# Kernel tuning notes

Measured on AMD Instinct MI355X. Metric: run time of the kernel, lower is better.

## Reference

```python
import jax, jax.numpy as jnp
import numpy as np

DIM = 512
HEADS = 8
HEAD_DIM = DIM // HEADS
EPS = 1e-6
LN_EPS = 1e-5


def setup_inputs() -> dict:
    key = jax.random.key(0)
    ks = jax.random.split(key, 7)
    B, S = 2, 2048
    std = 1.0 / np.sqrt(DIM)
    return {
        "x": jax.random.normal(ks[0], (B, S, DIM), dtype=jnp.float32),
        "Wq": jax.random.normal(ks[1], (DIM, DIM), dtype=jnp.float32) * std,
        "Wk": jax.random.normal(ks[2], (DIM, DIM), dtype=jnp.float32) * std,
        "Wv": jax.random.normal(ks[3], (DIM, DIM), dtype=jnp.float32) * std,
        "Wo": jax.random.normal(ks[4], (DIM, DIM), dtype=jnp.float32) * std,
        "ln_gamma": jnp.ones((DIM,), dtype=jnp.float32),
        "ln_beta": jnp.zeros((DIM,), dtype=jnp.float32),
    }


def _hardsigmoid(x):
    return jnp.clip(x / 6.0 + 0.5, 0.0, 1.0)


def _softshrink(x, lambd=0.5):
    return jnp.where(x > lambd, x - lambd, jnp.where(x < -lambd, x + lambd, 0.0))


def reference(x, Wq, Wk, Wv, Wo, ln_gamma, ln_beta):
    B, S, D = x.shape
    # torch Linear: y = x @ W.T
    q = (x @ Wq.T).reshape(B, S, HEADS, HEAD_DIM).transpose(0, 2, 1, 3)
    k = (x @ Wk.T).reshape(B, S, HEADS, HEAD_DIM).transpose(0, 2, 1, 3)
    v = (x @ Wv.T).reshape(B, S, HEADS, HEAD_DIM).transpose(0, 2, 1, 3)
    scale = 1.0 / np.sqrt(HEAD_DIM)
    scores = jnp.einsum("bhqd,bhkd->bhqk", q, k) * scale  # [B,H,S,S]
    attn_soft = jax.nn.softmax(scores, axis=-1)
    gated = attn_soft * _hardsigmoid(scores)
    attn_weights = gated / (gated.sum(axis=-1, keepdims=True) + EPS)
    attn_out = jnp.einsum("bhqk,bhkd->bhqd", attn_weights, v)
    attn_out = attn_out.transpose(0, 2, 1, 3).reshape(B, S, D)
    out = attn_out @ Wo.T
    out = out / (1.0 + jnp.abs(out))  # softsign
    out = out + _softshrink(x)
    # LayerNorm over last dim
    mu = out.mean(axis=-1, keepdims=True)
    var = ((out - mu) ** 2).mean(axis=-1, keepdims=True)
    out = (out - mu) * jax.lax.rsqrt(var + LN_EPS) * ln_gamma + ln_beta
    return out
```

## Files before the change

### kernel.cpp

```cpp
#include <hip/hip_runtime.h>

#define DIMD 512
#define NB 2
#define SEQ 2048
#define NHEADS 8
#define HDIM 64
#define MROWS (NB*SEQ)

typedef short s16x8 __attribute__((ext_vector_type(8)));
typedef float f32x4 __attribute__((ext_vector_type(4)));
typedef float f32x16 __attribute__((ext_vector_type(16)));
typedef unsigned short u16;
typedef unsigned int u32;

__device__ __forceinline__ u16 f2bf(float f) {
    union { float f; u32 u; } c; c.f = f;
    u32 u = c.u;
    return (u16)((u + 0x7FFFu + ((u >> 16) & 1u)) >> 16);
}
__device__ __forceinline__ float bf2f(u16 v) {
    union { u32 u; float f; } c; c.u = ((u32)v) << 16;
    return c.f;
}

__device__ __forceinline__ f32x4 mfma16(s16x8 a, s16x8 b, f32x4 c) {
    return __builtin_amdgcn_mfma_f32_16x16x32_bf16(a, b, c, 0, 0, 0);
}
__device__ __forceinline__ f32x16 mfma32(s16x8 a, s16x8 b, f32x16 c) {
    return __builtin_amdgcn_mfma_f32_32x32x16_bf16(a, b, c, 0, 0, 0);
}
__device__ __forceinline__ float fexp2(float x) {
    float r; asm("v_exp_f32 %0, %1" : "=v"(r) : "v"(x)); return r;
}

#define GLDS16(g, l) __builtin_amdgcn_global_load_lds( \
    (const __attribute__((address_space(1))) void*)(g), \
    (__attribute__((address_space(3))) void*)(l), 16, 0, 0)

#define ESCF 0.180336880111f
#define HSC2 0.115524530f

__global__ void cvt_all(const float* __restrict__ x, const float* __restrict__ Wq,
                        const float* __restrict__ Wk, const float* __restrict__ Wv,
                        const float* __restrict__ Wo,
                        u16* __restrict__ xb, u16* __restrict__ wqkv, u16* __restrict__ wo) {
    int i = blockIdx.x * blockDim.x + threadIdx.x;
    const float* src; u16* dst; int idx;
    if (i < 524288) { src = x; dst = xb; idx = i; }
    else {
        int jj = i - 524288;
        int which = jj >> 16; idx = jj & 65535;
        src = which == 0 ? Wq : which == 1 ? Wk : which == 2 ? Wv : Wo;
        dst = which < 3 ? wqkv + which*DIMD*DIMD : wo;
    }
    float4 v = reinterpret_cast<const float4*>(src)[idx];
    ushort4 o;
    o.x = f2bf(v.x); o.y = f2bf(v.y); o.z = f2bf(v.z); o.w = f2bf(v.w);
    reinterpret_cast<ushort4*>(dst)[idx] = o;
}

template<int WMODE>
__global__ __launch_bounds__(256) void gemm128(const u16* __restrict__ A, const u16* __restrict__ Bm,
                                               void* __restrict__ Cout, void* __restrict__ Cout2,
                                               void* __restrict__ Cout3, int M, int N, int K) {
    __shared__ u16 As[128*64];
    __shared__ u16 Bs[128*64];
    const int bm0 = blockIdx.x * 128, bn0 = blockIdx.y * 128;
    const int t = threadIdx.x;
    const int w = t >> 6, l = t & 63;
    const int lg = l >> 4, lr = l & 15;
    const int wm = w >> 1, wn = w & 1;
    f32x4 acc[4][4] = {};
    const int srow = w*32 + (l >> 3);
    const int swc = ((l & 7) ^ ((l >> 3) & 7)) * 8;
    const u16* asrc = A  + (size_t)(bm0 + srow)*K + swc;
    const u16* bsrc = Bm + (size_t)(bn0 + srow)*K + swc;
    const int ldsb = w*2048;

    for (int k0 = 0; k0 < K; k0 += 64) {
        #pragma unroll
        for (int g = 0; g < 4; g++) {
            GLDS16(asrc + (size_t)g*8*K + k0, &As[ldsb + g*512]);
            GLDS16(bsrc + (size_t)g*8*K + k0, &Bs[ldsb + g*512]);
        }
        __syncthreads();
        #pragma unroll
        for (int ks = 0; ks < 2; ks++) {
            const int swr = ((ks*4 + lg) ^ (lr & 7)) * 8;
            s16x8 af[4], bfr[4];
            #pragma unroll
            for (int fm = 0; fm < 4; fm++)
                af[fm] = *(const s16x8*)&As[(wm*64 + fm*16 + lr)*64 + swr];
            #pragma unroll
            for (int fn = 0; fn < 4; fn++)
                bfr[fn] = *(const s16x8*)&Bs[(wn*64 + fn*16 + lr)*64 + swr];
            #pragma unroll
            for (int fm = 0; fm < 4; fm++)
                #pragma unroll
                for (int fn = 0; fn < 4; fn++)
                    acc[fm][fn] = mfma16(af[fm], bfr[fn], acc[fm][fn]);
        }
        __syncthreads();
    }

    const int region = (WMODE == 3) ? (bn0 >> 9) : 0;
    const float qsc = (WMODE == 3 && region == 0) ? ESCF : 1.0f;
    #pragma unroll
    for (int fm = 0; fm < 4; fm++) {
        #pragma unroll
        for (int fn = 0; fn < 4; fn++) {
            const int mb = bm0 + wm*64 + fm*16 + lg*4;
            const int n  = bn0 + wn*64 + fn*16 + lr;
            if (WMODE == 2) {
                float* C = (float*)Cout;
                #pragma unroll
                for (int i = 0; i < 4; i++)
                    C[(size_t)(mb + i)*N + n] = acc[fm][fn][i];
            } else {
                const int nl = n & 511;
                if (region == 2) {
                    const int b = mb >> 11, s0 = mb & 2047;
                    const int h = nl >> 6, d = nl & 63;
                    ushort4 pk;
                    pk.x = f2bf(acc[fm][fn][0]);
                    pk.y = f2bf(acc[fm][fn][1]);
                    pk.z = f2bf(acc[fm][fn][2]);
                    pk.w = f2bf(acc[fm][fn][3]);
                    *(ushort4*)((u16*)Cout3 + (size_t)((b*8 + h)*64 + d)*2048 + s0) = pk;
                } else {
                    u16* C = region == 0 ? (u16*)Cout : (u16*)Cout2;
                    #pragma unroll
                    for (int i = 0; i < 4; i++)
                        C[(size_t)(mb + i)*512 + nl] = f2bf(acc[fm][fn][i] * qsc);
                }
            }
        }
    }
}

__global__ __launch_bounds__(256) void gemm_bt2(const u16* __restrict__ A, const u16* __restrict__ Bm,
                                                u16* __restrict__ Cout, int M, int N, int K) {
    __shared__ u16 As[64*64];
    __shared__ u16 Bs[64*64];
    const int bm0 = blockIdx.x * 64, bn0 = blockIdx.y * 64;
    const int t = threadIdx.x;
    const int w = t >> 6, l = t & 63;
    const int lg = l >> 4, lr = l & 15;
    const int wm = w >> 1, wn = w & 1;
    f32x4 acc[2][2] = {};
    const int srow = t >> 3;
    const int scol = (t & 7) * 8;

    for (int k0 = 0; k0 < K; k0 += 64) {
        #pragma unroll
        for (int c = 0; c < 2; c++) {
            const u16* ga = A  + (size_t)(bm0 + c*32 + srow)*K + k0 + scol;
            const u16* gb = Bm + (size_t)(bn0 + c*32 + srow)*K + k0 + scol;
            GLDS16(ga, (char*)As + c*4096 + w*1024);
            GLDS16(gb, (char*)Bs + c*4096 + w*1024);
        }
        __syncthreads();
        #pragma unroll
        for (int ks = 0; ks < 2; ks++) {
            s16x8 af[2], bfr[2];
            #pragma unroll
            for (int fm = 0; fm < 2; fm++)
                af[fm] = *(const s16x8*)&As[(wm*32 + fm*16 + lr)*64 + ks*32 + lg*8];
            #pragma unroll
            for (int fn = 0; fn < 2; fn++)
                bfr[fn] = *(const s16x8*)&Bs[(wn*32 + fn*16 + lr)*64 + ks*32 + lg*8];
            #pragma unroll
            for (int fm = 0; fm < 2; fm++)
                #pragma unroll
                for (int fn = 0; fn < 2; fn++)
                    acc[fm][fn] = mfma16(af[fm], bfr[fn], acc[fm][fn]);
        }
        __syncthreads();
    }

    #pragma unroll
    for (int fm = 0; fm < 2; fm++)
        #pragma unroll
        for (int fn = 0; fn < 2; fn++) {
            const int mb = bm0 + wm*32 + fm*16 + lg*4;
            const int n  = bn0 + wn*32 + fn*16 + lr;
            #pragma unroll
            for (int i = 0; i < 4; i++)
                Cout[(size_t)(mb + i)*N + n] = f2bf(acc[fm][fn][i]);
        }
}

__global__ __launch_bounds__(256) void attn_split(const u16* __restrict__ q, const u16* __restrict__ k,
                                                  const u16* __restrict__ vt,
                                                  u16* __restrict__ opart, float* __restrict__ gpart) {
    __shared__ u16 Ks[3][64*64];
    __shared__ u16 Vs[2][64*64];
    const int bid = blockIdx.x;
    const int xcd = bid & 7, j = bid >> 3;
    const int g8 = j >> 4, qt = j & 15;
    const int bhks = xcd*8 + g8;
    const int bh = bhks >> 2, ks = bhks & 3;
    const int b = bh >> 3, h = bh & 7;
    const int qb0 = qt * 128;
    const int t = threadIdx.x;
    const int w = t >> 6, l = t & 63;
    const int ln = l & 31, hi = l >> 5, l7 = l & 7;

    const size_t qrow = (size_t)(b*SEQ + qb0 + w*32 + ln);
    s16x8 qf[4];
    #pragma unroll
    for (int c = 0; c < 4; c++)
        qf[c] = *(const s16x8*)(q + qrow*DIMD + h*HDIM + c*16 + hi*8);

    const int sr = l >> 3;
    const int swc = ((l & 7) ^ sr) * 8;
    const u16* ksrc = k  + (size_t)(b*SEQ + ks*512 + w*16 + sr)*DIMD + h*HDIM + swc;
    const u16* vsrc = vt + (size_t)bh*HDIM*SEQ + (size_t)(w*16 + sr)*SEQ + ks*512 + swc;
    const int ldsw = w*1024;

    f32x16 o0 = {}, o1 = {};
    float gacc = 0.f;

#define SV(T, B) do { GLDS16(vsrc + (T)*64,                 &Vs[B][ldsw]); \
                      GLDS16(vsrc + (size_t)8*SEQ + (T)*64, &Vs[B][ldsw + 512]); } while(0)
#define SK(T, B) do { GLDS16(ksrc + (size_t)((T)*64)*DIMD,     &Ks[B][ldsw]); \
                      GLDS16(ksrc + (size_t)((T)*64 + 8)*DIMD, &Ks[B][ldsw + 512]); } while(0)
#define WB(N) do { asm volatile("s_waitcnt vmcnt(" #N ")" ::: "memory"); \
                   __builtin_amdgcn_s_barrier(); \
                   asm volatile("" ::: "memory"); } while(0)
#define QKH(B, KB, SC) do { SC = (f32x16){}; \
    __builtin_amdgcn_s_setprio(1); \
    _Pragma("unroll") for (int c_ = 0; c_ < 4; c_++) { \
        const int ch_ = (((c_ << 1) | hi) ^ l7) * 8; \
        s16x8 kf_ = *(const s16x8*)&Ks[B][((KB)*32 + ln)*64 + ch_]; \
        SC = mfma32(kf_, qf[c_], SC); } \
    __builtin_amdgcn_s_setprio(0); } while(0)
#define SMPV(SC, KB, VB) do { \
    u32 up_[4][2]; \
    _Pragma("unroll") for (int b2_ = 0; b2_ < 4; b2_++) { \
        const float s0_ = SC[b2_*4+0], s1_ = SC[b2_*4+1]; \
        const float s2_ = SC[b2_*4+2], s3_ = SC[b2_*4+3]; \
        const float w0_ = fexp2(s0_) * __builtin_amdgcn_fmed3f(s0_*HSC2 + 0.5f, 0.f, 1.f); \
        const float w1_ = fexp2(s1_) * __builtin_amdgcn_fmed3f(s1_*HSC2 + 0.5f, 0.f, 1.f); \
        const float w2_ = fexp2(s2_) * __builtin_amdgcn_fmed3f(s2_*HSC2 + 0.5f, 0.f, 1.f); \
        const float w3_ = fexp2(s3_) * __builtin_amdgcn_fmed3f(s3_*HSC2 + 0.5f, 0.f, 1.f); \
        gacc += (w0_ + w1_) + (w2_ + w3_); \
        asm("v_cvt_pk_bf16_f32 %0, %1, %2" : "=v"(up_[b2_][0]) : "v"(w0_), "v"(w1_)); \
        asm("v_cvt_pk_bf16_f32 %0, %1, %2" : "=v"(up_[b2_][1]) : "v"(w2_), "v"(w3_)); } \
    _Pragma("unroll") for (int c16_ = 0; c16_ < 2; c16_++) { \
        u32 x0_ = up_[2*c16_][0], y0_ = up_[2*c16_+1][0]; \
        u32 x1_ = up_[2*c16_][1], y1_ = up_[2*c16_+1][1]; \
        asm("v_permlane32_swap_b32 %0, %1" : "+v"(x0_), "+v"(y0_)); \
        asm("v_permlane32_swap_b32 %0, %1" : "+v"(x1_), "+v"(y1_)); \
        union { u32 w[4]; s16x8 v; } pa_; \
        pa_.w[0] = x0_; pa_.w[1] = x1_; pa_.w[2] = y0_; pa_.w[3] = y1_; \
        const int ccv_ = (KB)*4 + c16_*2 + hi; \
        s16x8 vf0_ = *(const s16x8*)&Vs[VB][(size_t)ln*64        + (ccv_ ^ l7)*8]; \
        s16x8 vf1_ = *(const s16x8*)&Vs[VB][(size_t)(32 + ln)*64 + (ccv_ ^ l7)*8]; \
        __builtin_amdgcn_s_setprio(1); \
        o0 = mfma32(pa_.v, vf0_, o0); \
        o1 = mfma32(pa_.v, vf1_, o1); \
        __builtin_amdgcn_s_setprio(0); } } while(0)

    f32x16 a0, a1, b0, b1;
    SV(0,0); SK(0,0); SK(1,1);
    WB(2);
    QKH(0,0,a0); SK(2,2); QKH(0,1,a1);
    WB(2);
    SV(1,1); QKH(1,0,b0); SK(3,0); SMPV(a0,0,0); QKH(1,1,b1); SMPV(a1,1,0);
    WB(2);
    SV(2,0); QKH(2,0,a0); SK(4,1); SMPV(b0,0,1); QKH(2,1,a1); SMPV(b1,1,1);
    WB(2);
    SV(3,1); QKH(0,0,b0); SK(5,2); SMPV(a0,0,0); QKH(0,1,b1); SMPV(a1,1,0);
    WB(2);
    SV(4,0); QKH(1,0,a0); SK(6,0); SMPV(b0,0,1); QKH(1,1,a1); SMPV(b1,1,1);
    WB(2);
    SV(5,1); QKH(2,0,b0); SK(7,1); SMPV(a0,0,0); QKH(2,1,b1); SMPV(a1,1,0);
    WB(2);
    SV(6,0); QKH(0,0,a0); SMPV(b0,0,1); QKH(0,1,a1); SMPV(b1,1,1);
    WB(0);
    SV(7,1); QKH(1,0,b0); SMPV(a0,0,0); QKH(1,1,b1); SMPV(a1,1,0);
    WB(0);
    SMPV(b0,0,1); SMPV(b1,1,1);

#undef SV
#undef SK
#undef WB
#undef QKH
#undef SMPV

    gacc += __shfl_xor(gacc, 32);
    if (l < 32)
        gpart[((size_t)ks*16 + bh)*SEQ + qb0 + w*32 + l] = gacc;

    u16* op = opart + ((size_t)ks*MROWS + b*SEQ + qb0 + w*32)*DIMD + h*HDIM;
    #pragma unroll
    for (int i = 0; i < 16; i++) {
        const int qr = (i & 3) + 8*(i >> 2) + 4*hi;
        op[(size_t)qr*DIMD + ln]      = f2bf(o0[i]);
        op[(size_t)qr*DIMD + 32 + ln] = f2bf(o1[i]);
    }
}

__global__ __launch_bounds__(256) void attn_combine(const u16* __restrict__ opart,
                                                    const float* __restrict__ gpart,
                                                    u16* __restrict__ attn) {
    const int idx = blockIdx.x*256 + threadIdx.x;
    const int row = idx >> 6;
    const int colb = (idx & 63) * 8;
    const int b = row >> 11, s = row & 2047, h = colb >> 6;
    float g = 0.f;
    #pragma unroll
    for (int p = 0; p < 4; p++)
        g += gpart[((size_t)p*16 + b*8 + h)*SEQ + s];
    const float inv = 1.f / g;
    float acc[8] = {};
    #pragma unroll
    for (int p = 0; p < 4; p++) {
        s16x8 v = *(const s16x8*)(opart + ((size_t)p*MROWS + row)*DIMD + colb);
        #pragma unroll
        for (int j2 = 0; j2 < 8; j2++) acc[j2] += bf2f((u16)v[j2]);
    }
    union { u16 r[8]; s16x8 v; } o;
    #pragma unroll
    for (int j2 = 0; j2 < 8; j2++) o.r[j2] = f2bf(acc[j2]*inv);
    *(s16x8*)(attn + (size_t)row*DIMD + colb) = o.v;
}

__global__ __launch_bounds__(256) void ln_epilogue(const u16* __restrict__ proj, const float* __restrict__ x,
                                                   const float* __restrict__ gamma, const float* __restrict__ beta,
                                                   float* __restrict__ out) {
    const int row = blockIdx.x*4 + (threadIdx.x >> 6);
    const int l = threadIdx.x & 63;
    const u16* pr = proj + (size_t)row*DIMD + l*8;
    const float* xr = x  + (size_t)row*DIMD + l*8;
    s16x8 pv = *(const s16x8*)pr;
    float tv[8];
    float s = 0.f, s2 = 0.f;
    #pragma unroll
    for (int j = 0; j < 2; j++) {
        float4 xv = *(const float4*)(xr + j*4);
        float xa[4] = {xv.x, xv.y, xv.z, xv.w};
        #pragma unroll
        for (int qq = 0; qq < 4; qq++) {
            const float p = bf2f((u16)pv[j*4+qq]);
            const float ss = p / (1.f + fabsf(p));
            const float xx = xa[qq];
            const float sh = xx > 0.5f ? xx - 0.5f : (xx < -0.5f ? xx + 0.5f : 0.f);
            const float tt = ss + sh;
            tv[j*4+qq] = tt; s += tt; s2 += tt*tt;
        }
    }
    #pragma unroll
    for (int m = 1; m < 64; m <<= 1) { s += __shfl_xor(s, m); s2 += __shfl_xor(s2, m); }
    const float mu = s * (1.f/512.f);
    float var = s2 * (1.f/512.f) - mu*mu;
    const float rstd = rsqrtf(var + 1e-5f);
    #pragma unroll
    for (int j = 0; j < 2; j++) {
        float4 g  = *(const float4*)(gamma + l*8 + j*4);
        float4 bb = *(const float4*)(beta  + l*8 + j*4);
        float4 ov;
        ov.x = (tv[j*4+0]-mu)*rstd*g.x + bb.x;
        ov.y = (tv[j*4+1]-mu)*rstd*g.y + bb.y;
        ov.z = (tv[j*4+2]-mu)*rstd*g.z + bb.z;
        ov.w = (tv[j*4+3]-mu)*rstd*g.w + bb.w;
        *(float4*)(out + (size_t)row*DIMD + l*8 + j*4) = ov;
    }
}

extern "C" void kernel_launch(void* const* d_in, const int* in_sizes, int n_in,
                              void* d_out, int out_size, void* d_ws, size_t ws_size,
                              hipStream_t stream) {
    const float* x     = (const float*)d_in[0];
    const float* Wq    = (const float*)d_in[1];
    const float* Wk    = (const float*)d_in[2];
    const float* Wv    = (const float*)d_in[3];
    const float* Wo    = (const float*)d_in[4];
    const float* gamma = (const float*)d_in[5];
    const float* beta  = (const float*)d_in[6];
    float* out = (float*)d_out;
    char* ws = (char*)d_ws;

    u16* xb    = (u16*)(ws);
    u16* wqkvb = (u16*)(ws + (4<<20));
    u16* wob   = (u16*)(ws + (4<<20) + (1536<<10));
    u16* qb    = (u16*)(ws + (6<<20));
    u16* kb    = (u16*)(ws + (10<<20));
    u16* vtb   = (u16*)(ws + (14<<20));
    u16* ab    = (u16*)(ws + (18<<20));
    u16* proj  = (u16*)(ws + (22<<20));
    u16* opart = (u16*)(ws + (26<<20));
    float* gpart = (float*)(ws + (42<<20));

    cvt_all<<<3072, 256, 0, stream>>>(x, Wq, Wk, Wv, Wo, xb, wqkvb, wob);

    gemm128<3><<<dim3(MROWS/128, 1536/128), 256, 0, stream>>>(xb, wqkvb, qb, kb, vtb, MROWS, 1536, DIMD);

    attn_split<<<1024, 256, 0, stream>>>(qb, kb, vtb, opart, gpart);
    attn_combine<<<1024, 256, 0, stream>>>(opart, gpart, ab);

    gemm_bt2<<<dim3(MROWS/64, DIMD/64), 256, 0, stream>>>(ab, wob, proj, MROWS, DIMD, DIMD);

    ln_epilogue<<<MROWS/4, 256, 0, stream>>>(proj, x, gamma, beta, out);
}
```

Measured before the change: 69.54 us.

## Fuse split-K attention combine into output projection GEMM A-tile load

```diff
diff --git a/kernel.cpp b/kernel.cpp
--- a/kernel.cpp
+++ b/kernel.cpp
@@ -31,6 +31,9 @@
 }
 __device__ __forceinline__ float fexp2(float x) {
     float r; asm("v_exp_f32 %0, %1" : "=v"(r) : "v"(x)); return r;
+}
+__device__ __forceinline__ float frcp(float x) {
+    float r; asm("v_rcp_f32 %0, %1" : "=v"(r) : "v"(x)); return r;
 }
 
 #define GLDS16(g, l) __builtin_amdgcn_global_load_lds( \
@@ -138,10 +141,13 @@
     }
 }
 
-__global__ __launch_bounds__(256) void gemm_bt2(const u16* __restrict__ A, const u16* __restrict__ Bm,
-                                                u16* __restrict__ Cout, int M, int N, int K) {
+__global__ __launch_bounds__(256) void gemm_bt2f(const u16* __restrict__ opart,
+                                                 const float* __restrict__ gpart,
+                                                 const u16* __restrict__ Bm,
+                                                 u16* __restrict__ Cout) {
     __shared__ u16 As[64*64];
     __shared__ u16 Bs[64*64];
+    __shared__ float ginv[64][9];
     const int bm0 = blockIdx.x * 64, bn0 = blockIdx.y * 64;
     const int t = threadIdx.x;
     const int w = t >> 6, l = t & 63;
@@ -149,26 +155,59 @@
     const int wm = w >> 1, wn = w & 1;
     f32x4 acc[2][2] = {};
     const int srow = t >> 3;
-    const int scol = (t & 7) * 8;
-
-    for (int k0 = 0; k0 < K; k0 += 64) {
+    const int c8 = t & 7;
+    const int scol = c8 * 8;
+    const int swz = (c8 ^ (srow & 7)) * 8;
+
+    #pragma unroll
+    for (int e = t; e < 512; e += 256) {
+        const int r = e >> 3, h = e & 7;
+        const int rg = bm0 + r;
+        const int b = rg >> 11, s = rg & 2047;
+        float g = gpart[(size_t)(b*8 + h)*SEQ + s]
+                + gpart[(size_t)(16 + b*8 + h)*SEQ + s]
+                + gpart[(size_t)(32 + b*8 + h)*SEQ + s]
+                + gpart[(size_t)(48 + b*8 + h)*SEQ + s];
+        ginv[r][h] = frcp(g);
+    }
+    __syncthreads();
+
+    for (int k0 = 0; k0 < DIMD; k0 += 64) {
+        const int h = k0 >> 6;
         #pragma unroll
         for (int c = 0; c < 2; c++) {
-            const u16* ga = A  + (size_t)(bm0 + c*32 + srow)*K + k0 + scol;
-            const u16* gb = Bm + (size_t)(bn0 + c*32 + srow)*K + k0 + scol;
-            GLDS16(ga, (char*)As + c*4096 + w*1024);
+            const int rl = c*32 + srow;
+            const int rg = bm0 + rl;
+            const u16* gb = Bm + (size_t)(bn0 + rl)*DIMD + k0 + swz;
             GLDS16(gb, (char*)Bs + c*4096 + w*1024);
+            const u16* oprow = opart + (size_t)rg*DIMD + k0 + scol;
+            s16x8 p0 = *(const s16x8*)(oprow);
+            s16x8 p1 = *(const s16x8*)(oprow + (size_t)MROWS*DIMD);
+            s16x8 p2 = *(const s16x8*)(oprow + (size_t)2*MROWS*DIMD);
+            s16x8 p3 = *(const s16x8*)(oprow + (size_t)3*MROWS*DIMD);
+            const float inv = ginv[rl][h];
+            union { u32 uu[4]; s16x8 v; } av;
+            #pragma unroll
+            for (int e2 = 0; e2 < 4; e2++) {
+                const float s0 = (bf2f((u16)p0[2*e2]) + bf2f((u16)p1[2*e2]))
+                               + (bf2f((u16)p2[2*e2]) + bf2f((u16)p3[2*e2]));
+                const float s1 = (bf2f((u16)p0[2*e2+1]) + bf2f((u16)p1[2*e2+1]))
+                               + (bf2f((u16)p2[2*e2+1]) + bf2f((u16)p3[2*e2+1]));
+                asm("v_cvt_pk_bf16_f32 %0, %1, %2" : "=v"(av.uu[e2]) : "v"(s0*inv), "v"(s1*inv));
+            }
+            *(s16x8*)&As[rl*64 + swz] = av.v;
         }
         __syncthreads();
         #pragma unroll
         for (int ks = 0; ks < 2; ks++) {
             s16x8 af[2], bfr[2];
+            const int rc = ((ks*4 + lg) ^ (lr & 7)) * 8;
             #pragma unroll
             for (int fm = 0; fm < 2; fm++)
-                af[fm] = *(const s16x8*)&As[(wm*32 + fm*16 + lr)*64 + ks*32 + lg*8];
+                af[fm] = *(const s16x8*)&As[(wm*32 + fm*16 + lr)*64 + rc];
             #pragma unroll
             for (int fn = 0; fn < 2; fn++)
-                bfr[fn] = *(const s16x8*)&Bs[(wn*32 + fn*16 + lr)*64 + ks*32 + lg*8];
+                bfr[fn] = *(const s16x8*)&Bs[(wn*32 + fn*16 + lr)*64 + rc];
             #pragma unroll
             for (int fm = 0; fm < 2; fm++)
                 #pragma unroll
@@ -186,7 +225,7 @@
             const int n  = bn0 + wn*32 + fn*16 + lr;
             #pragma unroll
             for (int i = 0; i < 4; i++)
-                Cout[(size_t)(mb + i)*N + n] = f2bf(acc[fm][fn][i]);
+                Cout[(size_t)(mb + i)*DIMD + n] = f2bf(acc[fm][fn][i]);
         }
 }
 
@@ -302,31 +341,6 @@
     }
 }
 
-__global__ __launch_bounds__(256) void attn_combine(const u16* __restrict__ opart,
-                                                    const float* __restrict__ gpart,
-                                                    u16* __restrict__ attn) {
-    const int idx = blockIdx.x*256 + threadIdx.x;
-    const int row = idx >> 6;
-    const int colb = (idx & 63) * 8;
-    const int b = row >> 11, s = row & 2047, h = colb >> 6;
-    float g = 0.f;
-    #pragma unroll
-    for (int p = 0; p < 4; p++)
-        g += gpart[((size_t)p*16 + b*8 + h)*SEQ + s];
-    const float inv = 1.f / g;
-    float acc[8] = {};
-    #pragma unroll
-    for (int p = 0; p < 4; p++) {
-        s16x8 v = *(const s16x8*)(opart + ((size_t)p*MROWS + row)*DIMD + colb);
-        #pragma unroll
-        for (int j2 = 0; j2 < 8; j2++) acc[j2] += bf2f((u16)v[j2]);
-    }
-    union { u16 r[8]; s16x8 v; } o;
-    #pragma unroll
-    for (int j2 = 0; j2 < 8; j2++) o.r[j2] = f2bf(acc[j2]*inv);
-    *(s16x8*)(attn + (size_t)row*DIMD + colb) = o.v;
-}
-
 __global__ __launch_bounds__(256) void ln_epilogue(const u16* __restrict__ proj, const float* __restrict__ x,
                                                    const float* __restrict__ gamma, const float* __restrict__ beta,
                                                    float* __restrict__ out) {
@@ -388,7 +402,6 @@
     u16* qb    = (u16*)(ws + (6<<20));
     u16* kb    = (u16*)(ws + (10<<20));
     u16* vtb   = (u16*)(ws + (14<<20));
-    u16* ab    = (u16*)(ws + (18<<20));
     u16* proj  = (u16*)(ws + (22<<20));
     u16* opart = (u16*)(ws + (26<<20));
     float* gpart = (float*)(ws + (42<<20));
@@ -398,9 +411,8 @@
     gemm128<3><<<dim3(MROWS/128, 1536/128), 256, 0, stream>>>(xb, wqkvb, qb, kb, vtb, MROWS, 1536, DIMD);
 
     attn_split<<<1024, 256, 0, stream>>>(qb, kb, vtb, opart, gpart);
-    attn_combine<<<1024, 256, 0, stream>>>(opart, gpart, ab);
-
-    gemm_bt2<<<dim3(MROWS/64, DIMD/64), 256, 0, stream>>>(ab, wob, proj, MROWS, DIMD, DIMD);
+
+    gemm_bt2f<<<dim3(MROWS/64, DIMD/64), 256, 0, stream>>>(opart, gpart, wob, proj);
 
     ln_epilogue<<<MROWS/4, 256, 0, stream>>>(proj, x, gamma, beta, out);
 }
```

Measured after the change: 68.53 us. About the same (-1.4%).
